# Kernel tuning notes

Hardware: AMD Instinct MI355X
Metric: run time of the kernel (lower is better)

Reference implementation:

```python
import jax, jax.numpy as jnp
import numpy as np

N_NODES = 50000
IN_CH = 256
Z_DIM = 64
N_EDGES = 800000


def setup_inputs() -> dict:
    key = jax.random.key(0)
    k_x, k_e, k_wm, k_ws = jax.random.split(key, 4)
    x = jax.random.normal(k_x, (N_NODES, IN_CH), dtype=jnp.float32)
    edge_index = jax.random.randint(k_e, (2, N_EDGES), 0, N_NODES, dtype=jnp.int64)
    # Glorot-style init like PyG GCNConv
    scale = 1.0 / np.sqrt(IN_CH)
    W_mu = jax.random.uniform(k_wm, (IN_CH, Z_DIM), dtype=jnp.float32, minval=-scale, maxval=scale)
    W_logstd = jax.random.uniform(k_ws, (IN_CH, Z_DIM), dtype=jnp.float32, minval=-scale, maxval=scale)
    b_mu = jnp.zeros((Z_DIM,), dtype=jnp.float32)
    b_logstd = jnp.zeros((Z_DIM,), dtype=jnp.float32)
    return {"x": x, "edge_index": edge_index, "W_mu": W_mu, "b_mu": b_mu,
            "W_logstd": W_logstd, "b_logstd": b_logstd}


def _gcn_conv(x, W, b, src, dst, deg_inv_sqrt, num_nodes):
    # PyG GCNConv: out = D^{-1/2} (A + I) D^{-1/2} X W + b
    xw = x @ W                                   # [N, Z]
    norm = deg_inv_sqrt[src] * deg_inv_sqrt[dst]  # [E+N]
    msg = xw[src] * norm[:, None]                 # gather + scale, [E+N, Z]
    agg = jax.ops.segment_sum(msg, dst, num_segments=num_nodes)  # scatter-add
    return agg + b


def reference(x, edge_index, W_mu, b_mu, W_logstd, b_logstd):
    num_nodes = x.shape[0]
    loops = jnp.arange(num_nodes, dtype=edge_index.dtype)
    src = jnp.concatenate([edge_index[0], loops])
    dst = jnp.concatenate([edge_index[1], loops])
    # degree (with self loops) on target nodes, symmetric normalization
    deg = jax.ops.segment_sum(jnp.ones_like(dst, dtype=x.dtype), dst, num_segments=num_nodes)
    deg_inv_sqrt = jnp.where(deg > 0, jax.lax.rsqrt(jnp.maximum(deg, 1.0)), 0.0)
    mu = _gcn_conv(x, W_mu, b_mu, src, dst, deg_inv_sqrt, num_nodes)
    logstd = _gcn_conv(x, W_logstd, b_logstd, src, dst, deg_inv_sqrt, num_nodes)
    return (mu, logstd)
```

## Files before the change

kernel.cpp:

```cpp
#include <hip/hip_runtime.h>

#define N_NODES 50000
#define IN_CH   256
#define Z_DIM   64
#define N_EDGES 800000
#define CH2     128
#define NODE_OFF (N_NODES * Z_DIM)
#define NBLK    ((N_NODES + 255) / 256)
#define SEG     8
#define SEGN    50048
#define NBUCKET (SEG * SEGN)
#define CAP     16
#define ECHUNKS (N_EDGES / 256)
#define NTILES  ((N_NODES + 31) / 32)
#define NW      32768

typedef __bf16 bf16x8 __attribute__((ext_vector_type(8)));
typedef float  f32x4  __attribute__((ext_vector_type(4)));

__device__ __forceinline__ unsigned short f2bf(float f) {
    __bf16 h = (__bf16)f;
    unsigned short u;
    __builtin_memcpy(&u, &h, 2);
    return u;
}
__device__ __forceinline__ float bf_lo(unsigned w) { return __uint_as_float(w << 16); }
__device__ __forceinline__ float bf_hi(unsigned w) { return __uint_as_float(w & 0xFFFF0000u); }

__global__ void k_pre(int* __restrict__ cur8,
                      const float* __restrict__ Wmu, const float* __restrict__ Wls,
                      unsigned short* __restrict__ WbT) {
    int g = blockIdx.x * 256 + threadIdx.x;
    if (g < NBUCKET) cur8[g] = 0;
    int h = g - NBUCKET;
    if (h >= 0 && h < NW) {
        int n = h >> 8, k = h & 255;
        float v = (n < 64) ? Wmu[(size_t)k * 64 + n] : Wls[(size_t)k * 64 + (n - 64)];
        WbT[(size_t)n * 256 + k] = f2bf(v);
    }
}

#define LDP  264
#define CSP2 136
__device__ __forceinline__ void gemm_tile(int t, const float* __restrict__ x,
                                          const unsigned short* __restrict__ WbT,
                                          unsigned short* __restrict__ xwb, char* smem) {
    unsigned short* As  = (unsigned short*)smem;
    unsigned short* Css = (unsigned short*)smem;
    const int tid = threadIdx.x;
    const int r0  = t * 32;

    {
        int row_l = tid >> 3;
        int cb    = (tid & 7) * 32;
        int row   = r0 + row_l;
        unsigned short* dp = As + row_l * LDP + cb;
        if (row < N_NODES) {
            const float4* xp = (const float4*)(x + (size_t)row * IN_CH + cb);
#pragma unroll
            for (int i = 0; i < 4; ++i) {
                float4 a = xp[2 * i];
                float4 b = xp[2 * i + 1];
                uint4 w;
                w.x = (unsigned)f2bf(a.x) | ((unsigned)f2bf(a.y) << 16);
                w.y = (unsigned)f2bf(a.z) | ((unsigned)f2bf(a.w) << 16);
                w.z = (unsigned)f2bf(b.x) | ((unsigned)f2bf(b.y) << 16);
                w.w = (unsigned)f2bf(b.z) | ((unsigned)f2bf(b.w) << 16);
                *(uint4*)(dp + i * 8) = w;
            }
        } else {
            uint4 z = make_uint4(0, 0, 0, 0);
#pragma unroll
            for (int i = 0; i < 4; ++i) *(uint4*)(dp + i * 8) = z;
        }
    }
    __syncthreads();

    const int wv   = tid >> 6;
    const int lane = tid & 63;
    const int m    = lane & 15;
    const int q    = lane >> 4;
    const int row_half = (wv & 1) * 16;
    const int col_half = (wv >> 1) * 64;

    f32x4 acc[4] = {};
    const unsigned short* ap = As + (row_half + m) * LDP + q * 8;
    const unsigned short* bp = WbT + (size_t)(col_half + m) * 256 + q * 8;

#pragma unroll
    for (int k0 = 0; k0 < IN_CH; k0 += 32) {
        bf16x8 af = *(const bf16x8*)(ap + k0);
#pragma unroll
        for (int nt = 0; nt < 4; ++nt) {
            bf16x8 bf_ = *(const bf16x8*)(bp + (size_t)nt * 16 * 256 + k0);
            acc[nt] = __builtin_amdgcn_mfma_f32_16x16x32_bf16(af, bf_, acc[nt], 0, 0, 0);
        }
    }

    __syncthreads();
#pragma unroll
    for (int nt = 0; nt < 4; ++nt)
#pragma unroll
        for (int r = 0; r < 4; ++r)
            Css[(row_half + q * 4 + r) * CSP2 + col_half + nt * 16 + m] = f2bf(acc[nt][r]);
    __syncthreads();

    {
        int row_l = tid >> 3;
        int c0    = (tid & 7) * 16;
        int row   = r0 + row_l;
        if (row < N_NODES) {
            const uint4* cp = (const uint4*)(Css + row_l * CSP2 + c0);
            uint4 w0 = cp[0];
            uint4 w1 = cp[1];
            uint4* op = (uint4*)(xwb + (size_t)row * CH2 + c0);
            op[0] = w0;
            op[1] = w1;
        }
    }
    __syncthreads();
}

__global__ __launch_bounds__(256) void k_gemm_scat(
    const float* __restrict__ x, const unsigned short* __restrict__ WbT,
    unsigned short* __restrict__ xwb,
    const int* __restrict__ src, const int* __restrict__ dst,
    int* __restrict__ cur8, unsigned short* __restrict__ pk2) {
    __shared__ __align__(16) char smem[32 * LDP * 2];
    if (blockIdx.x < NTILES) {
        gemm_tile(blockIdx.x, x, WbT, xwb, smem);
    } else {
        int c = blockIdx.x - NTILES;
        int e = c * 256 + threadIdx.x;
        int s = src[e];
        int d = dst[e];
        unsigned xcc;
        asm("s_getreg_b32 %0, hwreg(HW_REG_XCC_ID)" : "=s"(xcc));
        int seg = (int)(xcc & (SEG - 1));
        int idx = seg * SEGN + d;
        int pos = __hip_atomic_fetch_add(&cur8[idx], 1, __ATOMIC_RELAXED,
                                         __HIP_MEMORY_SCOPE_WORKGROUP);
        if (pos < CAP) pk2[(size_t)idx * CAP + pos] = (unsigned short)s;
    }
}

__global__ void k_dinv(const int* __restrict__ cur8, float* __restrict__ dinv) {
    int i = blockIdx.x * 256 + threadIdx.x;
    if (i >= N_NODES) return;
    int t = 1;
#pragma unroll
    for (int xg = 0; xg < SEG; ++xg) t += cur8[xg * SEGN + i];
    dinv[i] = rsqrtf((float)t);
}

#define PAIR(jj, pr)                                                          \
    if (2 * (jj) < cnt) {                                                     \
        int sa = (int)((pr) & 0xFFFFu);                                       \
        int sb = (int)((pr) >> 16);                                           \
        bool hb = (2 * (jj) + 1) < cnt;                                       \
        int sbe = hb ? sb : sa;                                               \
        float na = di * dinv[sa];                                             \
        float nb = hb ? di * dinv[sbe] : 0.f;                                 \
        const uint4 wa = *(const uint4*)(xwb + (size_t)sa * CH2 + cl * 8);    \
        const uint4 wb = *(const uint4*)(xwb + (size_t)sbe * CH2 + cl * 8);   \
        acc[0] += bf_lo(wa.x) * na + bf_lo(wb.x) * nb;                        \
        acc[1] += bf_hi(wa.x) * na + bf_hi(wb.x) * nb;                        \
        acc[2] += bf_lo(wa.y) * na + bf_lo(wb.y) * nb;                        \
        acc[3] += bf_hi(wa.y) * na + bf_hi(wb.y) * nb;                        \
        acc[4] += bf_lo(wa.z) * na + bf_lo(wb.z) * nb;                        \
        acc[5] += bf_hi(wa.z) * na + bf_hi(wb.z) * nb;                        \
        acc[6] += bf_lo(wa.w) * na + bf_lo(wb.w) * nb;                        \
        acc[7] += bf_hi(wa.w) * na + bf_hi(wb.w) * nb;                        \
    }

__global__ __launch_bounds__(256) void k_gather(const int* __restrict__ cur8,
                                                const unsigned short* __restrict__ pk2,
                                                const unsigned short* __restrict__ xwb,
                                                const float* __restrict__ dinv,
                                                const float* __restrict__ bmu,
                                                const float* __restrict__ bls,
                                                float* __restrict__ out) {
    const int i    = blockIdx.x * 4 + (threadIdx.x >> 6);
    const int lane = threadIdx.x & 63;
    const int q    = lane >> 4;
    const int cl   = lane & 15;

    float di = dinv[i];
    float acc[8] = {0.f, 0.f, 0.f, 0.f, 0.f, 0.f, 0.f, 0.f};
    if (q == 0) {
        float sq = di * di;
        uint4 w = *(const uint4*)(xwb + (size_t)i * CH2 + cl * 8);
        acc[0] = bf_lo(w.x) * sq; acc[1] = bf_hi(w.x) * sq;
        acc[2] = bf_lo(w.y) * sq; acc[3] = bf_hi(w.y) * sq;
        acc[4] = bf_lo(w.z) * sq; acc[5] = bf_hi(w.z) * sq;
        acc[6] = bf_lo(w.w) * sq; acc[7] = bf_hi(w.w) * sq;
    }

#pragma unroll
    for (int b = 0; b < 2; ++b) {
        const int idx = (q + b * 4) * SEGN + i;
        int cnt = cur8[idx];
        if (cnt > CAP) cnt = CAP;
        const uint4* pb = (const uint4*)(pk2 + (size_t)idx * CAP);
        const uint4 e0 = pb[0];
        const uint4 e1 = pb[1];
        PAIR(0, e0.x) PAIR(1, e0.y) PAIR(2, e0.z) PAIR(3, e0.w)
        PAIR(4, e1.x) PAIR(5, e1.y) PAIR(6, e1.z) PAIR(7, e1.w)
    }

#pragma unroll
    for (int k = 0; k < 8; ++k) {
        acc[k] += __shfl_xor(acc[k], 16);
        acc[k] += __shfl_xor(acc[k], 32);
    }

    if (lane < 16) {
        int c0 = cl * 8;
        const float* bb = (c0 < 64) ? (bmu + c0) : (bls + (c0 - 64));
        float4 b0 = *(const float4*)(bb + 0);
        float4 b1 = *(const float4*)(bb + 4);
        float* o = (c0 < 64) ? (out + (size_t)i * 64 + c0)
                             : (out + NODE_OFF + (size_t)i * 64 + (c0 - 64));
        *(float4*)(o + 0) = make_float4(acc[0] + b0.x, acc[1] + b0.y,
                                        acc[2] + b0.z, acc[3] + b0.w);
        *(float4*)(o + 4) = make_float4(acc[4] + b1.x, acc[5] + b1.y,
                                        acc[6] + b1.z, acc[7] + b1.w);
    }
}

extern "C" void kernel_launch(void* const* d_in, const int* in_sizes, int n_in,
                              void* d_out, int out_size, void* d_ws, size_t ws_size,
                              hipStream_t stream) {
    const float* x   = (const float*)d_in[0];
    const int*   ei  = (const int*)d_in[1];
    const float* Wmu = (const float*)d_in[2];
    const float* bmu = (const float*)d_in[3];
    const float* Wls = (const float*)d_in[4];
    const float* bls = (const float*)d_in[5];
    float* out = (float*)d_out;

    const int* src = ei;
    const int* dst = ei + N_EDGES;

    char* ws = (char*)d_ws;
    int*            cur8 = (int*)(ws + 0);
    float*          dinv = (float*)(ws + 1638400);
    unsigned short* WbT  = (unsigned short*)(ws + 1867776);
    unsigned short* pk2  = (unsigned short*)(ws + 2097152);
    unsigned short* xwb  = (unsigned short*)(ws + 16777216);

    k_pre<<<(NBUCKET + NW + 255) / 256, 256, 0, stream>>>(cur8, Wmu, Wls, WbT);
    k_gemm_scat<<<NTILES + ECHUNKS, 256, 0, stream>>>(x, WbT, xwb, src, dst, cur8, pk2);
    k_dinv<<<NBLK, 256, 0, stream>>>(cur8, dinv);
    k_gather<<<N_NODES / 4, 256, 0, stream>>>(cur8, pk2, xwb, dinv, bmu, bls, out);
}
```

Before: 211.2 us.

## Split fused GEMM/scatter kernel and enlarge GEMM tile to 128 rows with swizzled LDS

Separates the edge-bucketing scatter from the XW GEMM into two kernels launched back to back. The GEMM now processes 128-row tiles, with each wave computing 32 rows by 128 columns, which reuses each loaded B fragment across two A fragments. LDS rows are unpadded and use an XOR swizzle to avoid bank conflicts. The aim is better MFMA utilisation and less redundant reading of W. In exchange, the scatter and GEMM no longer overlap within a single launch, an extra launch is added, and the larger 64 KB LDS footprint limits occupancy.

```diff
diff --git a/kernel.cpp b/kernel.cpp
--- a/kernel.cpp
+++ b/kernel.cpp
@@ -12,7 +12,8 @@
 #define NBUCKET (SEG * SEGN)
 #define CAP     16
 #define ECHUNKS (N_EDGES / 256)
-#define NTILES  ((N_NODES + 31) / 32)
+#define TM      128
+#define GTILES  ((N_NODES + TM - 1) / TM)
 #define NW      32768
 
 typedef __bf16 bf16x8 __attribute__((ext_vector_type(8)));
@@ -40,107 +41,116 @@
     }
 }
 
-#define LDP  264
+__global__ __launch_bounds__(256) void k_scat(const int* __restrict__ src,
+                                              const int* __restrict__ dst,
+                                              int* __restrict__ cur8,
+                                              unsigned short* __restrict__ pk2) {
+    int e = blockIdx.x * 256 + threadIdx.x;
+    int s = src[e];
+    int d = dst[e];
+    unsigned xcc;
+    asm("s_getreg_b32 %0, hwreg(HW_REG_XCC_ID)" : "=s"(xcc));
+    int idx = (int)(xcc & (SEG - 1)) * SEGN + d;
+    int pos = __hip_atomic_fetch_add(&cur8[idx], 1, __ATOMIC_RELAXED,
+                                     __HIP_MEMORY_SCOPE_WORKGROUP);
+    if (pos < CAP) pk2[(size_t)idx * CAP + pos] = (unsigned short)s;
+}
+
 #define CSP2 136
-__device__ __forceinline__ void gemm_tile(int t, const float* __restrict__ x,
-                                          const unsigned short* __restrict__ WbT,
-                                          unsigned short* __restrict__ xwb, char* smem) {
-    unsigned short* As  = (unsigned short*)smem;
-    unsigned short* Css = (unsigned short*)smem;
+__global__ __launch_bounds__(256, 2) void k_gemm(const float* __restrict__ x,
+                                                 const unsigned short* __restrict__ WbT,
+                                                 unsigned short* __restrict__ xwb) {
+    __shared__ __align__(16) unsigned short As[TM * 256];
     const int tid = threadIdx.x;
-    const int r0  = t * 32;
+    const int r0  = blockIdx.x * TM;
 
     {
-        int row_l = tid >> 3;
-        int cb    = (tid & 7) * 32;
-        int row   = r0 + row_l;
-        unsigned short* dp = As + row_l * LDP + cb;
-        if (row < N_NODES) {
-            const float4* xp = (const float4*)(x + (size_t)row * IN_CH + cb);
-#pragma unroll
-            for (int i = 0; i < 4; ++i) {
-                float4 a = xp[2 * i];
-                float4 b = xp[2 * i + 1];
-                uint4 w;
-                w.x = (unsigned)f2bf(a.x) | ((unsigned)f2bf(a.y) << 16);
-                w.y = (unsigned)f2bf(a.z) | ((unsigned)f2bf(a.w) << 16);
-                w.z = (unsigned)f2bf(b.x) | ((unsigned)f2bf(b.y) << 16);
-                w.w = (unsigned)f2bf(b.z) | ((unsigned)f2bf(b.w) << 16);
-                *(uint4*)(dp + i * 8) = w;
+        int row_l0 = tid >> 3;
+        int cb     = (tid & 7) * 32;
+#pragma unroll
+        for (int r = 0; r < 4; ++r) {
+            int row_l = r * 32 + row_l0;
+            int row   = r0 + row_l;
+            char* dpb = (char*)As + row_l * 512;
+            unsigned cswz = (unsigned)((row_l & 7) << 4);
+            if (row < N_NODES) {
+                const float4* xp = (const float4*)(x + (size_t)row * IN_CH + cb);
+#pragma unroll
+                for (int i = 0; i < 4; ++i) {
+                    float4 a = xp[2 * i];
+                    float4 b = xp[2 * i + 1];
+                    uint4 w;
+                    w.x = (unsigned)f2bf(a.x) | ((unsigned)f2bf(a.y) << 16);
+                    w.y = (unsigned)f2bf(a.z) | ((unsigned)f2bf(a.w) << 16);
+                    w.z = (unsigned)f2bf(b.x) | ((unsigned)f2bf(b.y) << 16);
+                    w.w = (unsigned)f2bf(b.z) | ((unsigned)f2bf(b.w) << 16);
+                    *(uint4*)(dpb + (((unsigned)(cb * 2 + i * 16)) ^ cswz)) = w;
+                }
+            } else {
+                uint4 z = make_uint4(0, 0, 0, 0);
+#pragma unroll
+                for (int i = 0; i < 4; ++i)
+                    *(uint4*)(dpb + (((unsigned)(cb * 2 + i * 16)) ^ cswz)) = z;
             }
-        } else {
-            uint4 z = make_uint4(0, 0, 0, 0);
-#pragma unroll
-            for (int i = 0; i < 4; ++i) *(uint4*)(dp + i * 8) = z;
         }
     }
     __syncthreads();
 
-    const int wv   = tid >> 6;
-    const int lane = tid & 63;
-    const int m    = lane & 15;
-    const int q    = lane >> 4;
-    const int row_half = (wv & 1) * 16;
-    const int col_half = (wv >> 1) * 64;
-
-    f32x4 acc[4] = {};
-    const unsigned short* ap = As + (row_half + m) * LDP + q * 8;
-    const unsigned short* bp = WbT + (size_t)(col_half + m) * 256 + q * 8;
+    const int wv    = tid >> 6;
+    const int lane  = tid & 63;
+    const int m     = lane & 15;
+    const int q     = lane >> 4;
+    const int rbase = wv * 32;
+
+    f32x4 acc[2][8] = {};
+    const char* apb0 = (const char*)As + (rbase + m) * 512;
+    const char* apb1 = apb0 + 16 * 512;
+    const unsigned   sw  = (unsigned)((m & 7) << 4);
+    const unsigned short* bp = WbT + (size_t)m * 256 + q * 8;
 
 #pragma unroll
     for (int k0 = 0; k0 < IN_CH; k0 += 32) {
-        bf16x8 af = *(const bf16x8*)(ap + k0);
-#pragma unroll
-        for (int nt = 0; nt < 4; ++nt) {
+        unsigned off = ((unsigned)(q * 16 + 2 * k0)) ^ sw;
+        bf16x8 a0 = *(const bf16x8*)(apb0 + off);
+        bf16x8 a1 = *(const bf16x8*)(apb1 + off);
+#pragma unroll
+        for (int nt = 0; nt < 8; ++nt) {
             bf16x8 bf_ = *(const bf16x8*)(bp + (size_t)nt * 16 * 256 + k0);
-            acc[nt] = __builtin_amdgcn_mfma_f32_16x16x32_bf16(af, bf_, acc[nt], 0, 0, 0);
+            acc[0][nt] = __builtin_amdgcn_mfma_f32_16x16x32_bf16(a0, bf_, acc[0][nt], 0, 0, 0);
+            acc[1][nt] = __builtin_amdgcn_mfma_f32_16x16x32_bf16(a1, bf_, acc[1][nt], 0, 0, 0);
         }
     }
 
     __syncthreads();
-#pragma unroll
-    for (int nt = 0; nt < 4; ++nt)
-#pragma unroll
-        for (int r = 0; r < 4; ++r)
-            Css[(row_half + q * 4 + r) * CSP2 + col_half + nt * 16 + m] = f2bf(acc[nt][r]);
+    {
+        unsigned short* Css = As;
+#pragma unroll
+        for (int mi = 0; mi < 2; ++mi)
+#pragma unroll
+            for (int nt = 0; nt < 8; ++nt)
+#pragma unroll
+                for (int r = 0; r < 4; ++r)
+                    Css[(rbase + mi * 16 + q * 4 + r) * CSP2 + nt * 16 + m] =
+                        f2bf(acc[mi][nt][r]);
+    }
     __syncthreads();
-
     {
-        int row_l = tid >> 3;
-        int c0    = (tid & 7) * 16;
-        int row   = r0 + row_l;
-        if (row < N_NODES) {
-            const uint4* cp = (const uint4*)(Css + row_l * CSP2 + c0);
-            uint4 w0 = cp[0];
-            uint4 w1 = cp[1];
-            uint4* op = (uint4*)(xwb + (size_t)row * CH2 + c0);
-            op[0] = w0;
-            op[1] = w1;
+        int row_l = tid >> 2;
+        int c0    = (tid & 3) * 32;
+#pragma unroll
+        for (int rr = 0; rr < 2; ++rr) {
+            int rl  = rr * 64 + row_l;
+            int row = r0 + rl;
+            if (row < N_NODES) {
+                const uint4* cp = (const uint4*)(As + rl * CSP2 + c0);
+                uint4 w0 = cp[0];
+                uint4 w1 = cp[1];
+                uint4 w2 = cp[2];
+                uint4 w3 = cp[3];
+                uint4* op = (uint4*)(xwb + (size_t)row * CH2 + c0);
+                op[0] = w0; op[1] = w1; op[2] = w2; op[3] = w3;
+            }
         }
-    }
-    __syncthreads();
-}
-
-__global__ __launch_bounds__(256) void k_gemm_scat(
-    const float* __restrict__ x, const unsigned short* __restrict__ WbT,
-    unsigned short* __restrict__ xwb,
-    const int* __restrict__ src, const int* __restrict__ dst,
-    int* __restrict__ cur8, unsigned short* __restrict__ pk2) {
-    __shared__ __align__(16) char smem[32 * LDP * 2];
-    if (blockIdx.x < NTILES) {
-        gemm_tile(blockIdx.x, x, WbT, xwb, smem);
-    } else {
-        int c = blockIdx.x - NTILES;
-        int e = c * 256 + threadIdx.x;
-        int s = src[e];
-        int d = dst[e];
-        unsigned xcc;
-        asm("s_getreg_b32 %0, hwreg(HW_REG_XCC_ID)" : "=s"(xcc));
-        int seg = (int)(xcc & (SEG - 1));
-        int idx = seg * SEGN + d;
-        int pos = __hip_atomic_fetch_add(&cur8[idx], 1, __ATOMIC_RELAXED,
-                                         __HIP_MEMORY_SCOPE_WORKGROUP);
-        if (pos < CAP) pk2[(size_t)idx * CAP + pos] = (unsigned short)s;
     }
 }
 
@@ -250,7 +260,8 @@
     unsigned short* xwb  = (unsigned short*)(ws + 16777216);
 
     k_pre<<<(NBUCKET + NW + 255) / 256, 256, 0, stream>>>(cur8, Wmu, Wls, WbT);
-    k_gemm_scat<<<NTILES + ECHUNKS, 256, 0, stream>>>(x, WbT, xwb, src, dst, cur8, pk2);
+    k_scat<<<ECHUNKS, 256, 0, stream>>>(src, dst, cur8, pk2);
+    k_gemm<<<GTILES, 256, 0, stream>>>(x, WbT, xwb);
     k_dinv<<<NBLK, 256, 0, stream>>>(cur8, dinv);
     k_gather<<<N_NODES / 4, 256, 0, stream>>>(cur8, pk2, xwb, dinv, bmu, bls, out);
 }
```

After: 204.1 us. 3.4% less time.
